# Optimization experiments

Hardware: AMD Instinct MI355X
Metric: run time of the kernel (lower is better)

The kernel has to match this reference:

```python
import jax, jax.numpy as jnp
import numpy as np

B, S, DIN = 4, 2048, 1024
H, D = 16, 64  # num_head, per-head dim_out


def _xavier(key, shape):
    fan_in, fan_out = shape[0], shape[1]
    limit = float(np.sqrt(6.0 / (fan_in + fan_out)))
    return jax.random.uniform(key, shape, jnp.float32, -limit, limit)


def setup_inputs() -> dict:
    key = jax.random.key(0)
    k_x, k_q, k_k, k_v, k_o = jax.random.split(key, 5)
    inputs = jax.random.normal(k_x, (B, S, DIN), jnp.float32)
    # weights stored as [in, out] (transpose of torch Linear.weight); bias zeros
    return {
        "inputs": inputs,
        "wq": _xavier(k_q, (DIN, H * D)), "bq": jnp.zeros((H * D,), jnp.float32),
        "wk": _xavier(k_k, (DIN, H * D)), "bk": jnp.zeros((H * D,), jnp.float32),
        "wv": _xavier(k_v, (DIN, H * D)), "bv": jnp.zeros((H * D,), jnp.float32),
        "wo": _xavier(k_o, (H * D, D)),  "bo": jnp.zeros((D,), jnp.float32),
    }


def reference(inputs, wq, bq, wk, bk, wv, bv, wo, bo):
    b, s, _ = inputs.shape
    q = (inputs @ wq + bq).reshape(b, s, H, D).transpose(0, 2, 1, 3)  # bhsd
    k = (inputs @ wk + bk).reshape(b, s, H, D).transpose(0, 2, 1, 3)
    v = (inputs @ wv + bv).reshape(b, s, H, D).transpose(0, 2, 1, 3)
    scores = jnp.einsum('bhsd,bhSd->bhsS', q, k) / jnp.sqrt(jnp.float32(D))
    p = jax.nn.softmax(scores, axis=-1)
    o = jnp.einsum('bhsS,bhSd->bhsd', p, v)
    o = o.transpose(0, 2, 1, 3).reshape(b, s, H * D)
    return o @ wo + bo  # [b, s, D]
```

## Files before the change

### kernel.cpp

```cpp
#include <hip/hip_runtime.h>

typedef __attribute__((ext_vector_type(8))) __bf16 bf16x8;
typedef __attribute__((ext_vector_type(4))) float f32x4;

#define NB   4
#define NS   2048
#define NDIN 1024
#define NH   16
#define ND   64
#define NHD  1024
#define NM   (NB * NS)

__device__ __forceinline__ float bf2f(unsigned short u) {
    unsigned int x = ((unsigned int)u) << 16;
    return __builtin_bit_cast(float, x);
}
__device__ __forceinline__ unsigned short f2bf(float f) {
    unsigned int u = __builtin_bit_cast(unsigned int, f);
    u += 0x7fff + ((u >> 16) & 1);
    return (unsigned short)(u >> 16);
}
__device__ __forceinline__ unsigned int cvt_pk_bf16(float lo, float hi) {
    unsigned int r;
    asm("v_cvt_pk_bf16_f32 %0, %1, %2" : "=v"(r) : "v"(lo), "v"(hi));
    return r;
}
__device__ __forceinline__ void gload16(const unsigned short* g, unsigned short* l) {
    __builtin_amdgcn_global_load_lds((const __attribute__((address_space(1))) unsigned int*)g,
                                     (__attribute__((address_space(3))) unsigned int*)l, 16, 0, 0);
}

__global__ __launch_bounds__(256) void prep(
    const float* __restrict__ X, const float* __restrict__ wq,
    const float* __restrict__ wk, const float* __restrict__ wv,
    const float* __restrict__ wo, unsigned short* __restrict__ Xb,
    unsigned short* __restrict__ Wt, unsigned short* __restrict__ WoT) {
    __shared__ unsigned short t[32][33];
    int blk = blockIdx.x, tid = threadIdx.x;
    if (blk < 4096) {
        int i = blk * 256 + tid;
        float4 a = ((const float4*)X)[i * 2];
        float4 b = ((const float4*)X)[i * 2 + 1];
        union { uint4 u; unsigned short s[8]; } o;
        o.s[0] = f2bf(a.x); o.s[1] = f2bf(a.y); o.s[2] = f2bf(a.z); o.s[3] = f2bf(a.w);
        o.s[4] = f2bf(b.x); o.s[5] = f2bf(b.y); o.s[6] = f2bf(b.z); o.s[7] = f2bf(b.w);
        *(uint4*)(Xb + (size_t)i * 8) = o.u;
    } else if (blk < 4096 + 3072) {
        int bb = blk - 4096;
        int z = bb >> 10, rem = bb & 1023;
        const float* src = z == 0 ? wq : z == 1 ? wk : wv;
        unsigned short* dst = Wt + (size_t)z * 1024 * 1024;
        int k0 = (rem & 31) * 32, n0 = (rem >> 5) * 32;
        int tx = tid & 31, ty = tid >> 5;
#pragma unroll
        for (int i = 0; i < 32; i += 8)
            t[ty + i][tx] = f2bf(src[(size_t)(k0 + ty + i) * 1024 + (n0 + tx)]);
        __syncthreads();
#pragma unroll
        for (int i = 0; i < 32; i += 8)
            dst[(size_t)(n0 + ty + i) * 1024 + (k0 + tx)] = t[tx][ty + i];
    } else {
        int bb = blk - 7168;
        int k0 = (bb & 31) * 32, n0 = (bb >> 5) * 32;
        int tx = tid & 31, ty = tid >> 5;
#pragma unroll
        for (int i = 0; i < 32; i += 8)
            t[ty + i][tx] = f2bf(wo[(size_t)(k0 + ty + i) * 64 + (n0 + tx)]);
        __syncthreads();
#pragma unroll
        for (int i = 0; i < 32; i += 8)
            WoT[(size_t)(n0 + ty + i) * 1024 + (k0 + tx)] = t[tx][ty + i];
    }
}

__global__ __launch_bounds__(256) void gemm_qkv(
    const unsigned short* __restrict__ X, const unsigned short* __restrict__ Wt,
    const float* __restrict__ bq, const float* __restrict__ bk,
    const float* __restrict__ bv,
    unsigned short* __restrict__ Q, unsigned short* __restrict__ K,
    unsigned short* __restrict__ V) {
    __shared__ unsigned short smem[16384];

    int lin = blockIdx.x;
    int xcd = lin & 7, ii = lin >> 3;
    int mt = xcd * 8 + (ii & 7);
    int nt = ii >> 3;
    int mb = mt * 128, nb = nt * 128;

    int tid = threadIdx.x;
    int wid = tid >> 6, lane = tid & 63, quad = lane >> 4, l16 = lane & 15;
    int wm = (wid & 1) * 64, wn = (wid >> 1) * 64;

    int srow = 16 * wid + (lane >> 2);
    int scol = (lane & 3) * 8;
    const unsigned short* pa0 = X + (size_t)(mb + srow) * NDIN + scol;
    const unsigned short* pa1 = pa0 + (size_t)64 * NDIN;
    const unsigned short* pb0 = Wt + (size_t)(nb + srow) * NDIN + scol;
    const unsigned short* pb1 = pb0 + (size_t)64 * NDIN;

    auto stage = [&](int buf) {
        unsigned short* la = smem + buf * 8192 + wid * 512;
        unsigned short* lb = smem + buf * 8192 + 4096 + wid * 512;
        gload16(pa0, la);
        gload16(pa1, la + 2048);
        gload16(pb0, lb);
        gload16(pb1, lb + 2048);
        pa0 += 32; pa1 += 32; pb0 += 32; pb1 += 32;
    };

    f32x4 acc[4][4];
#pragma unroll
    for (int i = 0; i < 4; i++)
#pragma unroll
        for (int j = 0; j < 4; j++) acc[i][j] = (f32x4){0.f, 0.f, 0.f, 0.f};

    stage(0);
    __syncthreads();
    int cur = 0;
    for (int k0 = 0; k0 < NDIN; k0 += 32) {
        if (k0 + 32 < NDIN) stage(cur ^ 1);
        const unsigned short* Ab = smem + cur * 8192;
        const unsigned short* Bb = Ab + 4096;
        bf16x8 af[4], bfr[4];
#pragma unroll
        for (int i = 0; i < 4; i++)
            af[i] = *(const bf16x8*)(Ab + (wm + i * 16 + l16) * 32 + quad * 8);
#pragma unroll
        for (int j = 0; j < 4; j++)
            bfr[j] = *(const bf16x8*)(Bb + (wn + j * 16 + l16) * 32 + quad * 8);
#pragma unroll
        for (int i = 0; i < 4; i++)
#pragma unroll
            for (int j = 0; j < 4; j++)
                acc[i][j] = __builtin_amdgcn_mfma_f32_16x16x32_bf16(af[i], bfr[j], acc[i][j], 0, 0, 0);
        __syncthreads();
        cur ^= 1;
    }

    unsigned short (*Cl)[128] = (unsigned short (*)[128])smem;
    int wsel = nb >> 10;
    if (wsel < 2) {
        const float* bias = (wsel == 0) ? bq : bk;
        unsigned short* dstp = (wsel == 0) ? Q : K;
#pragma unroll
        for (int i = 0; i < 4; i++)
#pragma unroll
            for (int j = 0; j < 4; j++) {
                int nl = wn + j * 16 + l16;
                float bias_v = bias[(nb & 1023) + nl];
#pragma unroll
                for (int r = 0; r < 4; r++) {
                    int ml = wm + i * 16 + quad * 4 + r;
                    int pc = ((nl >> 3) ^ (ml & 15));
                    Cl[ml][(pc << 3) | (nl & 7)] = f2bf(acc[i][j][r] + bias_v);
                }
            }
        __syncthreads();
        int hl = tid >> 7, sl = tid & 127;
        int h = ((nb & 1023) >> 6) + hl;
        int m = mb + sl, b = m >> 11, sidx = m & 2047;
        unsigned short* orow = dstp + ((size_t)((b * NH + h) * NS + sidx)) * ND;
#pragma unroll
        for (int c = 0; c < 8; c++) {
            int pc = ((hl * 8 + c) ^ (sl & 15));
            *(uint4*)(orow + c * 8) = *(const uint4*)(&Cl[sl][pc << 3]);
        }
    } else {
#pragma unroll
        for (int i = 0; i < 4; i++)
#pragma unroll
            for (int j = 0; j < 4; j++) {
                int nl = wn + j * 16 + l16;
                float bias_v = bv[(nb & 1023) + nl];
#pragma unroll
                for (int r = 0; r < 4; r++) {
                    int pml = wm + (i >> 1) * 32 + quad * 8 + (i & 1) * 4 + r;
                    int pc = ((pml >> 3) ^ (nl & 15));
                    Cl[nl][(pc << 3) | (pml & 7)] = f2bf(acc[i][j][r] + bias_v);
                }
            }
        __syncthreads();
        int b = mb >> 11, smb = mb & 2047;
        int h0 = (nb & 1023) >> 6;
#pragma unroll
        for (int c = 0; c < 8; c++) {
            int o = c * 256 + tid;
            int row = o >> 4, sc = o & 15;
            int pc = sc ^ (row & 15);
            uint4 v = *(const uint4*)(&Cl[row][pc << 3]);
            int h = h0 + (row >> 6), d = row & 63;
            *(uint4*)(V + ((size_t)((b * NH + h) * ND + d)) * NS + smb + sc * 8) = v;
        }
    }
}

__global__ __launch_bounds__(256) void attn(
    const unsigned short* __restrict__ Q, const unsigned short* __restrict__ K,
    const unsigned short* __restrict__ VT, unsigned short* __restrict__ Obuf) {
    __shared__ unsigned short Kl[2][64][64];
    __shared__ unsigned short Vt[2][64][64];

    int lin = blockIdx.x;
    int xcd = lin & 7, idx = lin >> 3;
    int bh = ((idx >> 4) << 3) | xcd;
    int qt = idx & 15;

    size_t base = (size_t)bh * NS * ND;
    int tid = threadIdx.x, wid = tid >> 6, lane = tid & 63;
    int quad = lane >> 4, l16 = lane & 15;
    int lx = l16 & 7;
    int q0 = qt * 128 + wid * 32;

    bf16x8 qa[2][2];
#pragma unroll
    for (int s = 0; s < 2; s++)
#pragma unroll
        for (int f = 0; f < 2; f++) {
            union { uint4 u; unsigned short sv[8]; } in_, out_;
            in_.u = *(const uint4*)(Q + base + (size_t)(q0 + s * 16 + l16) * ND + f * 32 + quad * 8);
#pragma unroll
            for (int j = 0; j < 8; j++) out_.sv[j] = f2bf(bf2f(in_.sv[j]) * 0.125f);
            qa[s][f] = __builtin_bit_cast(bf16x8, out_.u);
        }

    float lrow[2] = {0.f, 0.f};
    f32x4 o[2][4];
#pragma unroll
    for (int s = 0; s < 2; s++)
#pragma unroll
        for (int t = 0; t < 4; t++) o[s][t] = (f32x4){0.f, 0.f, 0.f, 0.f};

    int r0 = wid * 16 + (lane >> 3), r1 = r0 + 8;
    int p0 = lane & 7;
    const unsigned short* kp0 = K + base + (size_t)r0 * ND + ((p0 ^ (r0 & 7)) * 8);
    const unsigned short* kp1 = K + base + (size_t)r1 * ND + ((p0 ^ (r1 & 7)) * 8);
    const unsigned short* vp0 = VT + base + (size_t)r0 * NS + ((p0 ^ (r0 & 7)) * 8);
    const unsigned short* vp1 = VT + base + (size_t)r1 * NS + ((p0 ^ (r1 & 7)) * 8);

    auto stageKV = [&](int buf) {
        unsigned short* kb = &Kl[buf][0][0] + wid * 1024;
        unsigned short* vb = &Vt[buf][0][0] + wid * 1024;
        gload16(kp0, kb);
        gload16(kp1, kb + 512);
        gload16(vp0, vb);
        gload16(vp1, vb + 512);
    };

    stageKV(0);
    __syncthreads();

    int cur = 0;
    for (int kc = 0; kc < NS; kc += 64) {
        bool more = (kc + 64 < NS);
        if (more) {
            kp0 += 64 * ND; kp1 += 64 * ND; vp0 += 64; vp1 += 64;
            stageKV(cur ^ 1);
        }

        f32x4 st[2][4];
        __builtin_amdgcn_s_setprio(1);
#pragma unroll
        for (int sub = 0; sub < 4; sub++) {
            const unsigned short* kr = &Kl[cur][sub * 16 + l16][0];
            bf16x8 kb0 = *(const bf16x8*)(kr + ((quad ^ lx) << 3));
            bf16x8 kb1 = *(const bf16x8*)(kr + (((4 + quad) ^ lx) << 3));
#pragma unroll
            for (int s = 0; s < 2; s++) {
                f32x4 c = (f32x4){0.f, 0.f, 0.f, 0.f};
                c = __builtin_amdgcn_mfma_f32_16x16x32_bf16(kb0, qa[s][0], c, 0, 0, 0);
                c = __builtin_amdgcn_mfma_f32_16x16x32_bf16(kb1, qa[s][1], c, 0, 0, 0);
                st[s][sub] = c;
            }
        }
        __builtin_amdgcn_s_setprio(0);

        bf16x8 pb[2][2];
#pragma unroll
        for (int s = 0; s < 2; s++) {
            float sum = 0.f;
#pragma unroll
            for (int sub = 0; sub < 4; sub++)
#pragma unroll
                for (int r = 0; r < 4; r++) {
                    float pv = __expf(st[s][sub][r]);
                    st[s][sub][r] = pv;
                    sum += pv;
                }
            lrow[s] += sum;
            unsigned int a0 = cvt_pk_bf16(st[s][0][0], st[s][0][1]);
            unsigned int a1 = cvt_pk_bf16(st[s][0][2], st[s][0][3]);
            unsigned int a2 = cvt_pk_bf16(st[s][1][0], st[s][1][1]);
            unsigned int a3 = cvt_pk_bf16(st[s][1][2], st[s][1][3]);
            pb[s][0] = __builtin_bit_cast(bf16x8, (uint4){a0, a1, a2, a3});
            unsigned int b0 = cvt_pk_bf16(st[s][2][0], st[s][2][1]);
            unsigned int b1 = cvt_pk_bf16(st[s][2][2], st[s][2][3]);
            unsigned int b2 = cvt_pk_bf16(st[s][3][0], st[s][3][1]);
            unsigned int b3 = cvt_pk_bf16(st[s][3][2], st[s][3][3]);
            pb[s][1] = __builtin_bit_cast(bf16x8, (uint4){b0, b1, b2, b3});
        }

        __builtin_amdgcn_s_setprio(1);
#pragma unroll
        for (int t = 0; t < 4; t++) {
            const unsigned short* vr = &Vt[cur][t * 16 + l16][0];
            bf16x8 vb0 = *(const bf16x8*)(vr + ((quad ^ lx) << 3));
            bf16x8 vb1 = *(const bf16x8*)(vr + (((4 + quad) ^ lx) << 3));
#pragma unroll
            for (int s = 0; s < 2; s++) {
                o[s][t] = __builtin_amdgcn_mfma_f32_16x16x32_bf16(vb0, pb[s][0], o[s][t], 0, 0, 0);
                o[s][t] = __builtin_amdgcn_mfma_f32_16x16x32_bf16(vb1, pb[s][1], o[s][t], 0, 0, 0);
            }
        }
        __builtin_amdgcn_s_setprio(0);

        __syncthreads();
        cur ^= 1;
    }

    int b = bh >> 4, h = bh & 15;
#pragma unroll
    for (int s = 0; s < 2; s++) {
        float ls = lrow[s];
        ls += __shfl_xor(ls, 16, 64);
        ls += __shfl_xor(ls, 32, 64);
        float inv = 1.0f / ls;
        int q = q0 + s * 16 + l16;
#pragma unroll
        for (int t = 0; t < 4; t++) {
            uint2 w;
            w.x = cvt_pk_bf16(o[s][t][0] * inv, o[s][t][1] * inv);
            w.y = cvt_pk_bf16(o[s][t][2] * inv, o[s][t][3] * inv);
            *(uint2*)(Obuf + (size_t)(b * NS + q) * NHD + h * ND + t * 16 + quad * 4) = w;
        }
    }
}

__global__ __launch_bounds__(256) void out_proj(
    const unsigned short* __restrict__ Obuf, const unsigned short* __restrict__ WoT,
    const float* __restrict__ bo, float* __restrict__ Out) {
    __shared__ float red[4][16][64];
    int m0 = blockIdx.x * 16;
    int tid = threadIdx.x, wid = tid >> 6, lane = tid & 63;
    int quad = lane >> 4, l16 = lane & 15;
    f32x4 acc[4];
#pragma unroll
    for (int t = 0; t < 4; t++) acc[t] = (f32x4){0.f, 0.f, 0.f, 0.f};
    int kb = wid * 256;
    for (int k0 = kb; k0 < kb + 256; k0 += 32) {
        bf16x8 a = *(const bf16x8*)(Obuf + (size_t)(m0 + l16) * NHD + k0 + quad * 8);
#pragma unroll
        for (int t = 0; t < 4; t++) {
            bf16x8 b = *(const bf16x8*)(WoT + (size_t)(t * 16 + l16) * NHD + k0 + quad * 8);
            acc[t] = __builtin_amdgcn_mfma_f32_16x16x32_bf16(a, b, acc[t], 0, 0, 0);
        }
    }
#pragma unroll
    for (int t = 0; t < 4; t++)
#pragma unroll
        for (int r = 0; r < 4; r++) red[wid][t * 4 + r][lane] = acc[t][r];
    __syncthreads();
    if (tid < 64) {
        int q2 = tid >> 4, s16 = tid & 15;
#pragma unroll
        for (int t = 0; t < 4; t++) {
            int n = t * 16 + s16;
            float bb = bo[n];
#pragma unroll
            for (int r = 0; r < 4; r++) {
                int idx = t * 4 + r;
                float v = red[0][idx][tid] + red[1][idx][tid] + red[2][idx][tid] + red[3][idx][tid];
                int m = m0 + q2 * 4 + r;
                Out[(size_t)m * ND + n] = v + bb;
            }
        }
    }
}

extern "C" void kernel_launch(void* const* d_in, const int* in_sizes, int n_in,
                              void* d_out, int out_size, void* d_ws, size_t ws_size,
                              hipStream_t stream) {
    const float* X  = (const float*)d_in[0];
    const float* wq = (const float*)d_in[1];
    const float* bq = (const float*)d_in[2];
    const float* wk = (const float*)d_in[3];
    const float* bk = (const float*)d_in[4];
    const float* wv = (const float*)d_in[5];
    const float* bv = (const float*)d_in[6];
    const float* wo = (const float*)d_in[7];
    const float* bo = (const float*)d_in[8];
    float* Out = (float*)d_out;

    char* w = (char*)d_ws;
    unsigned short* Wt  = (unsigned short*)w; w += (size_t)3072 * 1024 * 2;
    unsigned short* WoT = (unsigned short*)w; w += (size_t)64 * 1024 * 2;
    unsigned short* Xb  = (unsigned short*)w; w += (size_t)NM * NDIN * 2;
    unsigned short* Qb  = (unsigned short*)w; w += (size_t)NM * NHD * 2;
    unsigned short* Kb  = (unsigned short*)w; w += (size_t)NM * NHD * 2;
    unsigned short* Vb  = (unsigned short*)w; w += (size_t)NM * NHD * 2;
    unsigned short* Ob  = (unsigned short*)w; w += (size_t)NM * NHD * 2;

    prep<<<7232, 256, 0, stream>>>(X, wq, wk, wv, wo, Xb, Wt, WoT);
    gemm_qkv<<<1536, 256, 0, stream>>>(Xb, Wt, bq, bk, bv, Qb, Kb, Vb);
    attn<<<1024, 256, 0, stream>>>(Qb, Kb, Vb, Ob);
    out_proj<<<512, 256, 0, stream>>>(Ob, WoT, bo, Out);
}
```

Baseline: 280.6 us.

## Double attention query tile per wave to reuse K/V LDS fragments

Each wave of the attention kernel now handles 64 query rows instead of 32, so each block covers 256 queries and the grid shrinks from 1024 to 512 blocks. K and V fragments are read from LDS once per key chunk and reused across four query subtiles, with the softmax and PV product done per subtile. This halves total K/V global and LDS traffic per query, at the cost of more registers (launch bounds now ask for 2 blocks per CU) and fewer blocks to fill the GPU.

```diff
diff --git a/kernel.cpp b/kernel.cpp
--- a/kernel.cpp
+++ b/kernel.cpp
@@ -194,7 +194,7 @@
     }
 }
 
-__global__ __launch_bounds__(256) void attn(
+__global__ __launch_bounds__(256, 2) void attn(
     const unsigned short* __restrict__ Q, const unsigned short* __restrict__ K,
     const unsigned short* __restrict__ VT, unsigned short* __restrict__ Obuf) {
     __shared__ unsigned short Kl[2][64][64];
@@ -202,18 +202,18 @@
 
     int lin = blockIdx.x;
     int xcd = lin & 7, idx = lin >> 3;
-    int bh = ((idx >> 4) << 3) | xcd;
-    int qt = idx & 15;
+    int bh = ((idx >> 3) << 3) | xcd;
+    int qt = idx & 7;
 
     size_t base = (size_t)bh * NS * ND;
     int tid = threadIdx.x, wid = tid >> 6, lane = tid & 63;
     int quad = lane >> 4, l16 = lane & 15;
     int lx = l16 & 7;
-    int q0 = qt * 128 + wid * 32;
-
-    bf16x8 qa[2][2];
-#pragma unroll
-    for (int s = 0; s < 2; s++)
+    int q0 = qt * 256 + wid * 64;
+
+    bf16x8 qa[4][2];
+#pragma unroll
+    for (int s = 0; s < 4; s++)
 #pragma unroll
         for (int f = 0; f < 2; f++) {
             union { uint4 u; unsigned short sv[8]; } in_, out_;
@@ -223,10 +223,10 @@
             qa[s][f] = __builtin_bit_cast(bf16x8, out_.u);
         }
 
-    float lrow[2] = {0.f, 0.f};
-    f32x4 o[2][4];
-#pragma unroll
-    for (int s = 0; s < 2; s++)
+    float lrow[4] = {0.f, 0.f, 0.f, 0.f};
+    f32x4 o[4][4];
+#pragma unroll
+    for (int s = 0; s < 4; s++)
 #pragma unroll
         for (int t = 0; t < 4; t++) o[s][t] = (f32x4){0.f, 0.f, 0.f, 0.f};
 
@@ -257,61 +257,59 @@
             stageKV(cur ^ 1);
         }
 
-        f32x4 st[2][4];
-        __builtin_amdgcn_s_setprio(1);
-#pragma unroll
-        for (int sub = 0; sub < 4; sub++) {
-            const unsigned short* kr = &Kl[cur][sub * 16 + l16][0];
-            bf16x8 kb0 = *(const bf16x8*)(kr + ((quad ^ lx) << 3));
-            bf16x8 kb1 = *(const bf16x8*)(kr + (((4 + quad) ^ lx) << 3));
-#pragma unroll
-            for (int s = 0; s < 2; s++) {
+        bf16x8 kb[4][2], vb[4][2];
+#pragma unroll
+        for (int u = 0; u < 4; u++) {
+            const unsigned short* kr = &Kl[cur][u * 16 + l16][0];
+            kb[u][0] = *(const bf16x8*)(kr + ((quad ^ lx) << 3));
+            kb[u][1] = *(const bf16x8*)(kr + (((4 + quad) ^ lx) << 3));
+            const unsigned short* vr = &Vt[cur][u * 16 + l16][0];
+            vb[u][0] = *(const bf16x8*)(vr + ((quad ^ lx) << 3));
+            vb[u][1] = *(const bf16x8*)(vr + (((4 + quad) ^ lx) << 3));
+        }
+
+#pragma unroll
+        for (int s = 0; s < 4; s++) {
+            f32x4 st[4];
+            __builtin_amdgcn_s_setprio(1);
+#pragma unroll
+            for (int sub = 0; sub < 4; sub++) {
                 f32x4 c = (f32x4){0.f, 0.f, 0.f, 0.f};
-                c = __builtin_amdgcn_mfma_f32_16x16x32_bf16(kb0, qa[s][0], c, 0, 0, 0);
-                c = __builtin_amdgcn_mfma_f32_16x16x32_bf16(kb1, qa[s][1], c, 0, 0, 0);
-                st[s][sub] = c;
+                c = __builtin_amdgcn_mfma_f32_16x16x32_bf16(kb[sub][0], qa[s][0], c, 0, 0, 0);
+                c = __builtin_amdgcn_mfma_f32_16x16x32_bf16(kb[sub][1], qa[s][1], c, 0, 0, 0);
+                st[sub] = c;
             }
-        }
-        __builtin_amdgcn_s_setprio(0);
-
-        bf16x8 pb[2][2];
-#pragma unroll
-        for (int s = 0; s < 2; s++) {
+            __builtin_amdgcn_s_setprio(0);
+
             float sum = 0.f;
 #pragma unroll
             for (int sub = 0; sub < 4; sub++)
 #pragma unroll
                 for (int r = 0; r < 4; r++) {
-                    float pv = __expf(st[s][sub][r]);
-                    st[s][sub][r] = pv;
+                    float pv = __expf(st[sub][r]);
+                    st[sub][r] = pv;
                     sum += pv;
                 }
             lrow[s] += sum;
-            unsigned int a0 = cvt_pk_bf16(st[s][0][0], st[s][0][1]);
-            unsigned int a1 = cvt_pk_bf16(st[s][0][2], st[s][0][3]);
-            unsigned int a2 = cvt_pk_bf16(st[s][1][0], st[s][1][1]);
-            unsigned int a3 = cvt_pk_bf16(st[s][1][2], st[s][1][3]);
-            pb[s][0] = __builtin_bit_cast(bf16x8, (uint4){a0, a1, a2, a3});
-            unsigned int b0 = cvt_pk_bf16(st[s][2][0], st[s][2][1]);
-            unsigned int b1 = cvt_pk_bf16(st[s][2][2], st[s][2][3]);
-            unsigned int b2 = cvt_pk_bf16(st[s][3][0], st[s][3][1]);
-            unsigned int b3 = cvt_pk_bf16(st[s][3][2], st[s][3][3]);
-            pb[s][1] = __builtin_bit_cast(bf16x8, (uint4){b0, b1, b2, b3});
-        }
-
-        __builtin_amdgcn_s_setprio(1);
-#pragma unroll
-        for (int t = 0; t < 4; t++) {
-            const unsigned short* vr = &Vt[cur][t * 16 + l16][0];
-            bf16x8 vb0 = *(const bf16x8*)(vr + ((quad ^ lx) << 3));
-            bf16x8 vb1 = *(const bf16x8*)(vr + (((4 + quad) ^ lx) << 3));
-#pragma unroll
-            for (int s = 0; s < 2; s++) {
-                o[s][t] = __builtin_amdgcn_mfma_f32_16x16x32_bf16(vb0, pb[s][0], o[s][t], 0, 0, 0);
-                o[s][t] = __builtin_amdgcn_mfma_f32_16x16x32_bf16(vb1, pb[s][1], o[s][t], 0, 0, 0);
+            unsigned int a0 = cvt_pk_bf16(st[0][0], st[0][1]);
+            unsigned int a1 = cvt_pk_bf16(st[0][2], st[0][3]);
+            unsigned int a2 = cvt_pk_bf16(st[1][0], st[1][1]);
+            unsigned int a3 = cvt_pk_bf16(st[1][2], st[1][3]);
+            bf16x8 pb0 = __builtin_bit_cast(bf16x8, (uint4){a0, a1, a2, a3});
+            unsigned int b0 = cvt_pk_bf16(st[2][0], st[2][1]);
+            unsigned int b1 = cvt_pk_bf16(st[2][2], st[2][3]);
+            unsigned int b2 = cvt_pk_bf16(st[3][0], st[3][1]);
+            unsigned int b3 = cvt_pk_bf16(st[3][2], st[3][3]);
+            bf16x8 pb1 = __builtin_bit_cast(bf16x8, (uint4){b0, b1, b2, b3});
+
+            __builtin_amdgcn_s_setprio(1);
+#pragma unroll
+            for (int t = 0; t < 4; t++) {
+                o[s][t] = __builtin_amdgcn_mfma_f32_16x16x32_bf16(vb[t][0], pb0, o[s][t], 0, 0, 0);
+                o[s][t] = __builtin_amdgcn_mfma_f32_16x16x32_bf16(vb[t][1], pb1, o[s][t], 0, 0, 0);
             }
-        }
-        __builtin_amdgcn_s_setprio(0);
+            __builtin_amdgcn_s_setprio(0);
+        }
 
         __syncthreads();
         cur ^= 1;
@@ -319,7 +317,7 @@
 
     int b = bh >> 4, h = bh & 15;
 #pragma unroll
-    for (int s = 0; s < 2; s++) {
+    for (int s = 0; s < 4; s++) {
         float ls = lrow[s];
         ls += __shfl_xor(ls, 16, 64);
         ls += __shfl_xor(ls, 32, 64);
@@ -401,6 +399,6 @@
 
     prep<<<7232, 256, 0, stream>>>(X, wq, wk, wv, wo, Xb, Wt, WoT);
     gemm_qkv<<<1536, 256, 0, stream>>>(Xb, Wt, bq, bk, bv, Qb, Kb, Vb);
-    attn<<<1024, 256, 0, stream>>>(Qb, Kb, Vb, Ob);
+    attn<<<512, 256, 0, stream>>>(Qb, Kb, Vb, Ob);
     out_proj<<<512, 256, 0, stream>>>(Ob, WoT, bo, Out);
 }
```

Measured after the change: 247.4 us. 11.8% less time.
